# Kernel tuning notes

Measured on AMD Instinct MI355X. Metric: run time of the kernel, lower is better.

The kernel has to match this reference:

```python
import jax, jax.numpy as jnp
import numpy as np

KERNEL_LAM = 0.1


def setup_inputs() -> dict:
    key = jax.random.key(0)
    k1, k2, k3, k4 = jax.random.split(key, 4)
    B, H, L, C = 4, 1024, 4096, 1
    u = jax.random.normal(k1, (B, H, L), dtype=jnp.float32)
    kernel = jax.random.normal(k2, (C, H, 2 * L), dtype=jnp.float32) * 0.002
    D = jax.random.normal(k3, (C, H), dtype=jnp.float32)
    W = jax.random.normal(k4, (2 * H, C * H), dtype=jnp.float32) * (1.0 / np.sqrt(C * H))
    b = jnp.zeros((2 * H,), dtype=jnp.float32)
    return {"u": u, "kernel": kernel, "D": D, "W": W, "b": b}


def reference(u, kernel, D, W, b):
    B, H, L = u.shape
    n = 2 * L  # FFT length (kernel is length 2L)
    # soft-threshold the kernel
    k = jax.nn.relu(jnp.abs(kernel) - KERNEL_LAM) * jnp.sign(kernel)  # (C,H,2L)
    # FFT-based long convolution (flashfftconv equivalent): causal conv, take first L
    kf = jnp.fft.rfft(k, n=n)                       # (C,H,n//2+1)
    uf = jnp.fft.rfft(u, n=n)                       # (B,H,n//2+1)
    y = jnp.fft.irfft(uf[:, None] * kf[None], n=n)[..., :L]  # (B,C,H,L)
    # skip connection with D
    y = y + jnp.einsum('bhl,ch->bchl', u, D)
    # (B, C*H, L)
    y = y.reshape(B, -1, L)
    y = jax.nn.silu(y)
    # GLU projection over channel dim
    z = jnp.swapaxes(y, -1, -2) @ W.T + b           # (B,L,2H)
    a, g = jnp.split(z, 2, axis=-1)
    out = a * jax.nn.sigmoid(g)                     # (B,L,H)
    return jnp.swapaxes(out, -1, -2)                # (B,H,L)
```

## Files before the change

kernel.cpp:

```cpp
#include <hip/hip_runtime.h>
#include <stdint.h>

#define HD   1024
#define LD   4096
#define BATCH 4
#define KLEN 8192
#define LAM  0.1f
#define TAP_CAP 65536

typedef __attribute__((ext_vector_type(8))) short short8x;
typedef __attribute__((ext_vector_type(4))) float float4x;

struct Tap { int hd; float v; };

__device__ inline unsigned short f2bf(float x) {
    union { float f; uint32_t u; } v; v.f = x;
    uint32_t u = v.u;
    u += 0x7fffu + ((u >> 16) & 1u);
    return (unsigned short)(u >> 16);
}

__device__ inline void gload16(const void* g, void* l) {
    __builtin_amdgcn_global_load_lds(
        (const __attribute__((address_space(1))) void*)g,
        (__attribute__((address_space(3))) void*)l,
        16, 0, 0);
}

__device__ inline float silu_f(float x) { return x / (1.0f + __expf(-x)); }

__global__ void k_zero(int* p) {
    if (threadIdx.x < 16) p[threadIdx.x] = 0;
}

__global__ void k_scan(const float* __restrict__ kern, int* __restrict__ ntaps,
                       Tap* __restrict__ taps) {
    const float4* k4 = (const float4*)kern;
    int64_t total4 = (int64_t)HD * KLEN / 4;
    int64_t stride = (int64_t)gridDim.x * blockDim.x;
    for (int64_t i = blockIdx.x * blockDim.x + threadIdx.x; i < total4; i += stride) {
        float4 v = k4[i];
        float vals[4] = {v.x, v.y, v.z, v.w};
#pragma unroll
        for (int j = 0; j < 4; j++) {
            float a = fabsf(vals[j]) - LAM;
            if (a > 0.0f) {
                int e = (int)(i * 4 + j);
                int slot = atomicAdd(ntaps, 1);
                if (slot < TAP_CAP) { taps[slot].hd = e; taps[slot].v = copysignf(a, vals[j]); }
            }
        }
    }
}

__global__ void k_conv(const float* __restrict__ u, const float* __restrict__ Dv,
                       const int* __restrict__ ntaps_p, const Tap* __restrict__ taps,
                       float* __restrict__ yfull) {
    int nt = *ntaps_p;
    if (nt == 0) return;
    nt = min(nt, TAP_CAP);
    int64_t total = (int64_t)BATCH * HD * LD;
    int64_t stride = (int64_t)gridDim.x * blockDim.x;
    for (int64_t i = (int64_t)blockIdx.x * blockDim.x + threadIdx.x; i < total; i += stride) {
        int t = (int)(i & (LD - 1));
        int64_t bh = i >> 12;
        int h = (int)(bh & (HD - 1));
        float acc = u[i] * Dv[h];
        for (int j = 0; j < nt; j++) {
            int hd = taps[j].hd;
            if ((hd >> 13) != h) continue;
            int d = hd & (KLEN - 1);
            int s;
            if (d <= t) s = t - d;
            else { s = t - d + KLEN; if (s >= LD) continue; }
            acc += taps[j].v * u[(bh << 12) + s];
        }
        yfull[i] = acc;
    }
}

__global__ void k_wconv(const float* __restrict__ W, unsigned short* __restrict__ Wbf) {
    int i = blockIdx.x * 256 + threadIdx.x;
    const float4* w4 = (const float4*)W;
    float4 a = w4[i * 2], b = w4[i * 2 + 1];
    short8x o;
    o[0] = (short)f2bf(a.x); o[1] = (short)f2bf(a.y);
    o[2] = (short)f2bf(a.z); o[3] = (short)f2bf(a.w);
    o[4] = (short)f2bf(b.x); o[5] = (short)f2bf(b.y);
    o[6] = (short)f2bf(b.z); o[7] = (short)f2bf(b.w);
    *(short8x*)(Wbf + (int64_t)i * 8) = o;
}

__global__ __launch_bounds__(256) void k_vt(const float* __restrict__ u,
                                            const float* __restrict__ Dv,
                                            const float* __restrict__ yfull,
                                            const int* __restrict__ ntaps_p,
                                            unsigned short* __restrict__ Vt) {
    __shared__ float T[64][68];
    int nt = *ntaps_p;
    int lt = blockIdx.x * 64;
    int ht = blockIdx.y * 64;
    int b  = blockIdx.z;
    int tid = threadIdx.x;
    int lq = tid & 15;
    int hh = tid >> 4;
#pragma unroll
    for (int r = 0; r < 4; r++) {
        int h = hh + r * 16;
        int hg = ht + h;
        int64_t base = ((int64_t)b * HD + hg) * LD + lt + lq * 4;
        float4 v;
        if (nt == 0) {
            v = *(const float4*)(u + base);
            float d = Dv[hg];
            v.x *= d; v.y *= d; v.z *= d; v.w *= d;
        } else {
            v = *(const float4*)(yfull + base);
        }
        v.x = silu_f(v.x); v.y = silu_f(v.y); v.z = silu_f(v.z); v.w = silu_f(v.w);
        *(float4*)&T[h][lq * 4] = v;
    }
    __syncthreads();
    int l  = tid & 63;
    int hc = tid >> 6;
#pragma unroll
    for (int oc = 0; oc < 2; oc++) {
        int h8 = (hc + oc * 4) * 8;
        short8x o;
#pragma unroll
        for (int j = 0; j < 8; j++) o[j] = (short)f2bf(T[h8 + j][l]);
        int64_t n = (int64_t)b * LD + lt + l;
        *(short8x*)(Vt + n * HD + ht + h8) = o;
    }
}

__global__ __launch_bounds__(256, 2) void k_gemm(const unsigned short* __restrict__ Wbf,
                                                 const unsigned short* __restrict__ Vt,
                                                 const float* __restrict__ bvec,
                                                 float* __restrict__ out) {
    __shared__ unsigned short smem[12288];
    int m0 = blockIdx.x * 128;
    int n0 = blockIdx.y * 128;
    int tid = threadIdx.x;

    const unsigned short* gsrc[6];
    unsigned short* ldst[6];
#pragma unroll
    for (int i = 0; i < 6; i++) {
        int c = tid + i * 256;
        ldst[i] = smem + c * 8;
        if (c < 1024) {
            int r = c >> 2, kc = c & 3;
            int grow = (r < 128) ? (m0 + r) : (1024 + m0 + (r - 128));
            gsrc[i] = Wbf + (int64_t)grow * HD + kc * 8;
        } else {
            int cc = c - 1024;
            int col = cc >> 2, kc = cc & 3;
            gsrc[i] = Vt + (int64_t)(n0 + col) * HD + kc * 8;
        }
    }

    int lane = tid & 63;
    int wid  = tid >> 6;
    int wm = wid >> 1, wn = wid & 1;
    int l15 = lane & 15, quad = lane >> 4;

    int aoff[4], goff[4], boff[4];
#pragma unroll
    for (int i = 0; i < 4; i++) {
        int ra = wm * 64 + i * 16 + l15;
        aoff[i] = ra * 32 + quad * 8;
        goff[i] = (128 + ra) * 32 + quad * 8;
        int cb = wn * 64 + i * 16 + l15;
        boff[i] = 8192 + cb * 32 + quad * 8;
    }

    float4x acca[4][4], accg[4][4];
#pragma unroll
    for (int i = 0; i < 4; i++)
#pragma unroll
        for (int j = 0; j < 4; j++) {
            acca[i][j] = (float4x){0.f, 0.f, 0.f, 0.f};
            accg[i][j] = (float4x){0.f, 0.f, 0.f, 0.f};
        }

    for (int kt = 0; kt < 32; kt++) {
#pragma unroll
        for (int i = 0; i < 6; i++) gload16(gsrc[i], ldst[i]);
#pragma unroll
        for (int i = 0; i < 6; i++) gsrc[i] += 32;
        __syncthreads();
        short8x af[4], gf[4], bf[4];
#pragma unroll
        for (int i = 0; i < 4; i++) {
            af[i] = *(const short8x*)(smem + aoff[i]);
            gf[i] = *(const short8x*)(smem + goff[i]);
            bf[i] = *(const short8x*)(smem + boff[i]);
        }
#pragma unroll
        for (int i = 0; i < 4; i++)
#pragma unroll
            for (int j = 0; j < 4; j++) {
                acca[i][j] = __builtin_amdgcn_mfma_f32_16x16x32_bf16(af[i], bf[j], acca[i][j], 0, 0, 0);
                accg[i][j] = __builtin_amdgcn_mfma_f32_16x16x32_bf16(gf[i], bf[j], accg[i][j], 0, 0, 0);
            }
        __syncthreads();
    }

    int b = n0 >> 12;
#pragma unroll
    for (int i = 0; i < 4; i++) {
        int h = m0 + wm * 64 + i * 16 + quad * 4;
#pragma unroll
        for (int j = 0; j < 4; j++) {
            int n = n0 + wn * 64 + j * 16 + l15;
            int l = n & (LD - 1);
            float* op = out + ((int64_t)b * HD + h) * LD + l;
#pragma unroll
            for (int r = 0; r < 4; r++) {
                float av = acca[i][j][r] + bvec[h + r];
                float gv = accg[i][j][r] + bvec[1024 + h + r];
                op[(int64_t)r * LD] = av / (1.0f + __expf(-gv));
            }
        }
    }
}

extern "C" void kernel_launch(void* const* d_in, const int* in_sizes, int n_in,
                              void* d_out, int out_size, void* d_ws, size_t ws_size,
                              hipStream_t stream) {
    const float* u    = (const float*)d_in[0];
    const float* kern = (const float*)d_in[1];
    const float* Dv   = (const float*)d_in[2];
    const float* W    = (const float*)d_in[3];
    const float* bv   = (const float*)d_in[4];
    float* out = (float*)d_out;

    char* ws = (char*)d_ws;
    int* ntaps = (int*)ws;
    Tap* taps  = (Tap*)(ws + 256);
    unsigned short* Wbf = (unsigned short*)(ws + (1 << 20));
    unsigned short* Vt  = (unsigned short*)(ws + (8 << 20));
    float* yfull = (float*)(ws + (40 << 20));

    hipLaunchKernelGGL(k_zero,  dim3(1),          dim3(64),  0, stream, ntaps);
    hipLaunchKernelGGL(k_scan,  dim3(2048),       dim3(256), 0, stream, kern, ntaps, taps);
    hipLaunchKernelGGL(k_conv,  dim3(1024),       dim3(256), 0, stream, u, Dv, ntaps, taps, yfull);
    hipLaunchKernelGGL(k_wconv, dim3(1024),       dim3(256), 0, stream, W, Wbf);
    hipLaunchKernelGGL(k_vt,    dim3(64, 16, 4),  dim3(256), 0, stream, u, Dv, yfull, ntaps, Vt);
    hipLaunchKernelGGL(k_gemm,  dim3(8, 128),     dim3(256), 0, stream, Wbf, Vt, bv, out);
}
```

Measured before the change: 244.9 us.

## Fuse prep kernels, swizzle GEMM LDS, remap blocks per XCD, fix transpose banks

Merges the bf16 weight conversion and the kernel tap scan into one launch and replaces the zeroing kernel with a memset. The GEMM's LDS layout gets an XOR swizzle on the K-chunk slot to reduce bank conflicts, and a 1D grid remaps blocks so that N tiles are grouped per XCD for L2 reuse. The transpose kernel switches to stride-65 padding with a different read pattern, the bias loads are hoisted out of the epilogue loop, and the conv grid is halved. These are several independent changes aimed at launch overhead, LDS conflicts and cache locality.

```diff
diff --git a/kernel.cpp b/kernel.cpp
--- a/kernel.cpp
+++ b/kernel.cpp
@@ -29,16 +29,26 @@
 
 __device__ inline float silu_f(float x) { return x / (1.0f + __expf(-x)); }
 
-__global__ void k_zero(int* p) {
-    if (threadIdx.x < 16) p[threadIdx.x] = 0;
-}
-
-__global__ void k_scan(const float* __restrict__ kern, int* __restrict__ ntaps,
-                       Tap* __restrict__ taps) {
+__global__ void k_prep(const float* __restrict__ kern, int* __restrict__ ntaps,
+                       Tap* __restrict__ taps,
+                       const float* __restrict__ W, unsigned short* __restrict__ Wbf) {
+    if (blockIdx.x < 1024) {
+        int i = blockIdx.x * 256 + threadIdx.x;
+        const float4* w4 = (const float4*)W;
+        float4 a = w4[i * 2], b = w4[i * 2 + 1];
+        short8x o;
+        o[0] = (short)f2bf(a.x); o[1] = (short)f2bf(a.y);
+        o[2] = (short)f2bf(a.z); o[3] = (short)f2bf(a.w);
+        o[4] = (short)f2bf(b.x); o[5] = (short)f2bf(b.y);
+        o[6] = (short)f2bf(b.z); o[7] = (short)f2bf(b.w);
+        *(short8x*)(Wbf + (int64_t)i * 8) = o;
+        return;
+    }
+    int bid = blockIdx.x - 1024;
     const float4* k4 = (const float4*)kern;
     int64_t total4 = (int64_t)HD * KLEN / 4;
-    int64_t stride = (int64_t)gridDim.x * blockDim.x;
-    for (int64_t i = blockIdx.x * blockDim.x + threadIdx.x; i < total4; i += stride) {
+    int64_t stride = (int64_t)2048 * 256;
+    for (int64_t i = (int64_t)bid * 256 + threadIdx.x; i < total4; i += stride) {
         float4 v = k4[i];
         float vals[4] = {v.x, v.y, v.z, v.w};
 #pragma unroll
@@ -79,24 +89,12 @@
     }
 }
 
-__global__ void k_wconv(const float* __restrict__ W, unsigned short* __restrict__ Wbf) {
-    int i = blockIdx.x * 256 + threadIdx.x;
-    const float4* w4 = (const float4*)W;
-    float4 a = w4[i * 2], b = w4[i * 2 + 1];
-    short8x o;
-    o[0] = (short)f2bf(a.x); o[1] = (short)f2bf(a.y);
-    o[2] = (short)f2bf(a.z); o[3] = (short)f2bf(a.w);
-    o[4] = (short)f2bf(b.x); o[5] = (short)f2bf(b.y);
-    o[6] = (short)f2bf(b.z); o[7] = (short)f2bf(b.w);
-    *(short8x*)(Wbf + (int64_t)i * 8) = o;
-}
-
 __global__ __launch_bounds__(256) void k_vt(const float* __restrict__ u,
                                             const float* __restrict__ Dv,
                                             const float* __restrict__ yfull,
                                             const int* __restrict__ ntaps_p,
                                             unsigned short* __restrict__ Vt) {
-    __shared__ float T[64][68];
+    __shared__ float T[64 * 65];
     int nt = *ntaps_p;
     int lt = blockIdx.x * 64;
     int ht = blockIdx.y * 64;
@@ -117,19 +115,22 @@
         } else {
             v = *(const float4*)(yfull + base);
         }
-        v.x = silu_f(v.x); v.y = silu_f(v.y); v.z = silu_f(v.z); v.w = silu_f(v.w);
-        *(float4*)&T[h][lq * 4] = v;
+        int p = h * 65 + lq * 4;
+        T[p]     = silu_f(v.x);
+        T[p + 1] = silu_f(v.y);
+        T[p + 2] = silu_f(v.z);
+        T[p + 3] = silu_f(v.w);
     }
     __syncthreads();
-    int l  = tid & 63;
-    int hc = tid >> 6;
-#pragma unroll
-    for (int oc = 0; oc < 2; oc++) {
-        int h8 = (hc + oc * 4) * 8;
+    int h8 = (tid & 7) * 8;
+    int nb = tid >> 3;
+#pragma unroll
+    for (int p = 0; p < 2; p++) {
+        int nl = nb + p * 32;
         short8x o;
 #pragma unroll
-        for (int j = 0; j < 8; j++) o[j] = (short)f2bf(T[h8 + j][l]);
-        int64_t n = (int64_t)b * LD + lt + l;
+        for (int j = 0; j < 8; j++) o[j] = (short)f2bf(T[(h8 + j) * 65 + nl]);
+        int64_t n = (int64_t)b * LD + lt + nl;
         *(short8x*)(Vt + n * HD + ht + h8) = o;
     }
 }
@@ -139,8 +140,13 @@
                                                  const float* __restrict__ bvec,
                                                  float* __restrict__ out) {
     __shared__ unsigned short smem[12288];
-    int m0 = blockIdx.x * 128;
-    int n0 = blockIdx.y * 128;
+    int f   = blockIdx.x;
+    int xcd = f & 7;
+    int s   = f >> 3;
+    int ngrp = xcd * 16 + (s & 15);
+    int mgrp = s >> 4;
+    int m0 = mgrp * 128;
+    int n0 = ngrp * 128;
     int tid = threadIdx.x;
 
     const unsigned short* gsrc[6];
@@ -150,13 +156,15 @@
         int c = tid + i * 256;
         ldst[i] = smem + c * 8;
         if (c < 1024) {
-            int r = c >> 2, kc = c & 3;
+            int r = c >> 2, slot = c & 3;
+            int kg = slot ^ (r & 3);
             int grow = (r < 128) ? (m0 + r) : (1024 + m0 + (r - 128));
-            gsrc[i] = Wbf + (int64_t)grow * HD + kc * 8;
+            gsrc[i] = Wbf + (int64_t)grow * HD + kg * 8;
         } else {
             int cc = c - 1024;
-            int col = cc >> 2, kc = cc & 3;
-            gsrc[i] = Vt + (int64_t)(n0 + col) * HD + kc * 8;
+            int col = cc >> 2, slot = cc & 3;
+            int kg = slot ^ (col & 3);
+            gsrc[i] = Vt + (int64_t)(n0 + col) * HD + kg * 8;
         }
     }
 
@@ -164,15 +172,16 @@
     int wid  = tid >> 6;
     int wm = wid >> 1, wn = wid & 1;
     int l15 = lane & 15, quad = lane >> 4;
+    int kq = quad ^ (l15 & 3);
 
     int aoff[4], goff[4], boff[4];
 #pragma unroll
     for (int i = 0; i < 4; i++) {
         int ra = wm * 64 + i * 16 + l15;
-        aoff[i] = ra * 32 + quad * 8;
-        goff[i] = (128 + ra) * 32 + quad * 8;
+        aoff[i] = ra * 32 + kq * 8;
+        goff[i] = (128 + ra) * 32 + kq * 8;
         int cb = wn * 64 + i * 16 + l15;
-        boff[i] = 8192 + cb * 32 + quad * 8;
+        boff[i] = 8192 + cb * 32 + kq * 8;
     }
 
     float4x acca[4][4], accg[4][4];
@@ -211,6 +220,9 @@
 #pragma unroll
     for (int i = 0; i < 4; i++) {
         int h = m0 + wm * 64 + i * 16 + quad * 4;
+        float ba[4], bg[4];
+#pragma unroll
+        for (int r = 0; r < 4; r++) { ba[r] = bvec[h + r]; bg[r] = bvec[1024 + h + r]; }
 #pragma unroll
         for (int j = 0; j < 4; j++) {
             int n = n0 + wn * 64 + j * 16 + l15;
@@ -218,8 +230,8 @@
             float* op = out + ((int64_t)b * HD + h) * LD + l;
 #pragma unroll
             for (int r = 0; r < 4; r++) {
-                float av = acca[i][j][r] + bvec[h + r];
-                float gv = accg[i][j][r] + bvec[1024 + h + r];
+                float av = acca[i][j][r] + ba[r];
+                float gv = accg[i][j][r] + bg[r];
                 op[(int64_t)r * LD] = av / (1.0f + __expf(-gv));
             }
         }
@@ -243,10 +255,9 @@
     unsigned short* Vt  = (unsigned short*)(ws + (8 << 20));
     float* yfull = (float*)(ws + (40 << 20));
 
-    hipLaunchKernelGGL(k_zero,  dim3(1),          dim3(64),  0, stream, ntaps);
-    hipLaunchKernelGGL(k_scan,  dim3(2048),       dim3(256), 0, stream, kern, ntaps, taps);
-    hipLaunchKernelGGL(k_conv,  dim3(1024),       dim3(256), 0, stream, u, Dv, ntaps, taps, yfull);
-    hipLaunchKernelGGL(k_wconv, dim3(1024),       dim3(256), 0, stream, W, Wbf);
-    hipLaunchKernelGGL(k_vt,    dim3(64, 16, 4),  dim3(256), 0, stream, u, Dv, yfull, ntaps, Vt);
-    hipLaunchKernelGGL(k_gemm,  dim3(8, 128),     dim3(256), 0, stream, Wbf, Vt, bv, out);
-}
+    hipMemsetAsync(ntaps, 0, 256, stream);
+    hipLaunchKernelGGL(k_prep, dim3(3072),      dim3(256), 0, stream, kern, ntaps, taps, W, (unsigned short*)Wbf);
+    hipLaunchKernelGGL(k_conv, dim3(512),       dim3(256), 0, stream, u, Dv, ntaps, taps, yfull);
+    hipLaunchKernelGGL(k_vt,   dim3(64, 16, 4), dim3(256), 0, stream, u, Dv, yfull, ntaps, Vt);
+    hipLaunchKernelGGL(k_gemm, dim3(1024),      dim3(256), 0, stream, Wbf, Vt, bv, out);
+}
```

Result: faster. 233.8 us (-4.5%).
